# Kernel optimization log

Measured on AMD Instinct MI355X. Metric: run time of the kernel, lower is better.

The kernel has to match this reference:

```python
import jax, jax.numpy as jnp
import numpy as np

B, S, H = 64, 512, 256
H2 = 2 * H
TOPK, TRUNC = 5, 100
EPS = 1e-7
TMAX = S + 1  # h_old slot 0 is the initial zero state; one slot appended per step
NEG = -1e9


def setup_inputs() -> dict:
    key = jax.random.key(0)
    ks = jax.random.split(key, 8)
    p = lambda k, shape: jax.random.normal(k, shape, jnp.float32) * 0.08
    return {
        "x": jax.random.normal(ks[0], (B, S), jnp.float32),
        "W_ih_f": p(ks[1], (4 * H, 1)),
        "W_hh_f": p(ks[2], (4 * H, H)),
        "b_f": p(ks[3], (4 * H,)),
        "W_ih_b": p(ks[4], (4 * H, 1)),
        "W_hh_b": p(ks[5], (4 * H, H)),
        "b_b": p(ks[6], (4 * H,)),
        "w_t": p(ks[7], (4 * H, 1)),
    }


def _lstm_cell(xt, h, c, W_ih, W_hh, b):
    # torch.nn.LSTMCell: gates ordered i, f, g, o
    g = xt @ W_ih.T + h @ W_hh.T + b
    i, f, gg, o = jnp.split(g, 4, axis=1)
    i, f, o = jax.nn.sigmoid(i), jax.nn.sigmoid(f), jax.nn.sigmoid(o)
    c2 = f * c + i * jnp.tanh(gg)
    return o * jnp.tanh(c2), c2


def _forward(x, W_ih_f, W_hh_f, b_f, W_ih_b, W_hh_b, b_b, w_t):
    # tanh(cat(h_comb, h_old)) @ w_t == tanh(h_comb)@w1 + tanh(h_old)@w2
    w1, w2 = w_t[:H2, 0], w_t[H2:, 0]
    pos = jnp.arange(TMAX)

    h0 = jnp.zeros((B, H), jnp.float32)
    h_old0 = jnp.zeros((B, TMAX, H2), jnp.float32)   # slot 0 = initial zeros (valid)
    th_old0 = jnp.zeros((B, TMAX, H2), jnp.float32)  # cached tanh(h_old)
    carry0 = (h0, h0, h0, h0, h_old0, th_old0,
              jnp.zeros((B, H2), jnp.float32), jnp.zeros((B, TMAX), jnp.float32))

    def step(carry, i):
        h_f, c_f, h_b, c_b, h_old, th_old, _, _ = carry
        trunc = ((i + 1) % TRUNC) == 0  # TBPTT detach point
        sg = lambda a: jnp.where(trunc, jax.lax.stop_gradient(a), a)
        h_f, c_f, h_b, c_b = sg(h_f), sg(c_f), sg(h_b), sg(c_b)

        xf = jax.lax.dynamic_slice_in_dim(x, i, 1, axis=1)          # [B,1]
        xb = jax.lax.dynamic_slice_in_dim(x, S - 1 - i, 1, axis=1)  # [B,1]
        h_f, c_f = _lstm_cell(xf, h_f, c_f, W_ih_f, W_hh_f, b_f)
        h_b, c_b = _lstm_cell(xb, h_b, c_b, W_ih_b, W_hh_b, b_b)
        h_comb = jnp.concatenate([h_f, h_b], axis=1)  # [B,2H]

        rs = i + 1                    # remember_size before append
        valid = pos < rs              # [TMAX]
        s = jnp.tanh(h_comb) @ w1[:, None] + th_old @ w2  # [B,1]+[B,TMAX]
        s_m = jnp.where(valid[None, :], s, NEG)

        # Sparse_attention: subtract k-th largest, clamp at 0, renormalize
        delta = jax.lax.top_k(s_m, TOPK)[0][:, -1] + EPS  # [B]
        w_sp = jnp.clip(s_m - delta[:, None], 0.0, None)
        w_sp = w_sp / (w_sp.sum(axis=1, keepdims=True) + EPS)
        w_raw = jnp.where(valid[None, :], s, 0.0)  # time_step <= top_k branch
        attn_w = jnp.where(rs <= TOPK, w_raw, w_sp)  # [B,TMAX]

        attn_c = jnp.einsum('bt,bth->bh', attn_w, h_old)  # weighted sum of cache
        h_new = h_comb + attn_c

        h_old = jax.lax.dynamic_update_slice_in_dim(
            h_old, h_new[:, None, :], i + 1, axis=1)
        th_old = jax.lax.dynamic_update_slice_in_dim(
            th_old, jnp.tanh(h_new)[:, None, :], i + 1, axis=1)
        return (h_f, c_f, h_b, c_b, h_old, th_old, attn_c, attn_w), None

    carry, _ = jax.lax.scan(step, carry0, jnp.arange(S))
    attn_c, attn_w = carry[6], carry[7]
    # last step: remember_size == S, torch returns [B, S, 1]
    return attn_c, attn_w[:, :S, None]


def reference(x, W_ih_f, W_hh_f, b_f, W_ih_b, W_hh_b, b_b, w_t):
    return _forward(x, W_ih_f, W_hh_f, b_f, W_ih_b, W_hh_b, b_b, w_t)
```

## Files before the change

kernel.cpp:

```cpp
#include <hip/hip_runtime.h>
#include <math.h>

#define BB    64
#define SS    512
#define HH    256
#define HH2   512
#define TMAXX 513
#define NTOP  5
#define EPSF  1e-7f

#if defined(__has_builtin)
#if __has_builtin(__builtin_amdgcn_sdot4)
#define HAVE_SDOT4 1
#endif
#endif

__device__ __forceinline__ int dot4i8_(unsigned a, int b, int c) {
#ifdef HAVE_SDOT4
  return __builtin_amdgcn_sdot4((int)a, b, c, false);
#else
  int acc = c;
#pragma unroll
  for (int j = 0; j < 4; ++j) {
    int av = (int)(signed char)(a >> (8 * j));
    int bv = (int)(signed char)(((unsigned)b) >> (8 * j));
    acc += av * bv;
  }
  return acc;
#endif
}


__global__ void init_kernel(const float* __restrict__ Whh_f, const float* __restrict__ Whh_b,
                            uint4* __restrict__ wq, float* __restrict__ scales) {
  int t = blockIdx.x * blockDim.x + threadIdx.x;
  if (t >= 2048) return;
  int d = t >> 10, row = t & 1023;
  const float* src = (d ? Whh_b : Whh_f) + (size_t)row * HH;
  float m = 1e-20f;
  for (int k = 0; k < HH; ++k) m = fmaxf(m, fabsf(src[k]));
  float inv = 127.f / m;
  scales[t] = m * (1.f / 16129.f);
  for (int kq4 = 0; kq4 < 16; ++kq4) {
    unsigned u[4];
#pragma unroll
    for (int w = 0; w < 4; ++w) {
      unsigned uu = 0;
#pragma unroll
      for (int j = 0; j < 4; ++j) {
        float q = rintf(src[kq4 * 16 + w * 4 + j] * inv);
        q = fminf(fmaxf(q, -127.f), 127.f);
        uu |= ((unsigned)(((int)q) & 0xff)) << (8 * j);
      }
      u[w] = uu;
    }
    wq[(size_t)(d * 16 + kq4) * 1024 + row] = make_uint4(u[0], u[1], u[2], u[3]);
  }
}

__global__ __launch_bounds__(256, 1)
void lstm_kernel(const float* __restrict__ x,
                 const float* __restrict__ wihf, const float* __restrict__ bf,
                 const float* __restrict__ wihb, const float* __restrict__ bb_,
                 const uint4* __restrict__ wq, const float* __restrict__ scales,
                 float* __restrict__ hcomb) {
  const int r = blockIdx.x >> 1;
  const int d = blockIdx.x & 1;
  const int e = threadIdx.x;

  __shared__ float x_lds[SS];
  __shared__ int   hbuf[2][64];

  for (int t = e; t < SS; t += 256) x_lds[t] = x[(size_t)r * SS + t];
  if (e < 64) hbuf[0][e] = 0;

  float wih[4], bias[4], sc[4];
#pragma unroll
  for (int g = 0; g < 4; ++g) {
    int row = g * HH + e;
    wih[g]  = d ? wihb[row] : wihf[row];
    bias[g] = d ? bb_[row]  : bf[row];
    sc[g]   = scales[d * 1024 + row];
  }
  uint4 w[4][16];
#pragma unroll
  for (int g = 0; g < 4; ++g) {
    const uint4* wb = wq + (size_t)(d * 16) * 1024 + g * HH + e;
#pragma unroll
    for (int q = 0; q < 16; ++q) w[g][q] = wb[(size_t)q * 1024];
  }
  float c = 0.f;
  float* hout = hcomb + (size_t)r * SS * HH2 + d * HH;
  __syncthreads();

  int cur = 0;
  for (int i = 0; i < SS; ++i) {
    const int4* hp = (const int4*)hbuf[cur];
    int a0 = 0, a1 = 0, a2 = 0, a3 = 0;
#pragma unroll
    for (int q = 0; q < 16; ++q) {
      int4 h4 = hp[q];
      a0 = dot4i8_(w[0][q].x, h4.x, a0); a0 = dot4i8_(w[0][q].y, h4.y, a0);
      a0 = dot4i8_(w[0][q].z, h4.z, a0); a0 = dot4i8_(w[0][q].w, h4.w, a0);
      a1 = dot4i8_(w[1][q].x, h4.x, a1); a1 = dot4i8_(w[1][q].y, h4.y, a1);
      a1 = dot4i8_(w[1][q].z, h4.z, a1); a1 = dot4i8_(w[1][q].w, h4.w, a1);
      a2 = dot4i8_(w[2][q].x, h4.x, a2); a2 = dot4i8_(w[2][q].y, h4.y, a2);
      a2 = dot4i8_(w[2][q].z, h4.z, a2); a2 = dot4i8_(w[2][q].w, h4.w, a2);
      a3 = dot4i8_(w[3][q].x, h4.x, a3); a3 = dot4i8_(w[3][q].y, h4.y, a3);
      a3 = dot4i8_(w[3][q].z, h4.z, a3); a3 = dot4i8_(w[3][q].w, h4.w, a3);
    }
    float xv = x_lds[d ? (SS - 1 - i) : i];
    float gi = (float)a0 * sc[0] + fmaf(xv, wih[0], bias[0]);
    float gf = (float)a1 * sc[1] + fmaf(xv, wih[1], bias[1]);
    float gg = (float)a2 * sc[2] + fmaf(xv, wih[2], bias[2]);
    float go = (float)a3 * sc[3] + fmaf(xv, wih[3], bias[3]);
    float ig = 1.f / (1.f + expf(-gi));
    float fg = 1.f / (1.f + expf(-gf));
    float og = 1.f / (1.f + expf(-go));
    c = fg * c + ig * tanhf(gg);
    float hn = og * tanhf(c);
    hout[(size_t)i * HH2 + e] = hn;
    ((signed char*)hbuf[cur ^ 1])[e] = (signed char)(int)rintf(hn * 127.f);
    cur ^= 1;
    __syncthreads();
  }
}

__global__ __launch_bounds__(64, 1)
void attn_kernel(const float* __restrict__ w_t, const float* __restrict__ hcomb,
                 float* __restrict__ out) {
  const int b = blockIdx.x;
  const int l = threadIdx.x;
  const float* hrow = hcomb + (size_t)b * SS * HH2;

  __shared__ float tw_l[TMAXX];

  const float4 w1a = *(const float4*)(w_t + 4 * l);
  const float4 w1b = *(const float4*)(w_t + HH + 4 * l);
  const float4 w2a = *(const float4*)(w_t + HH2 + 4 * l);
  const float4 w2b = *(const float4*)(w_t + HH2 + HH + 4 * l);

  float t5v[5] = {0.f, -1e30f, -1e30f, -1e30f, -1e30f};
  int   t5s[5] = {0, 1, 2, 3, 4};
  int   t5cnt  = 1;
  float4 z4 = make_float4(0.f, 0.f, 0.f, 0.f);
  float4 sA0 = z4, sA1 = z4, sA2 = z4, sA3 = z4, sA4 = z4;
  float4 sB0 = z4, sB1 = z4, sB2 = z4, sB3 = z4, sB4 = z4;
  if (l == 0) tw_l[0] = 0.f;

  float4 ha = *(const float4*)(hrow + 4 * l);
  float4 hb = *(const float4*)(hrow + HH + 4 * l);
  float tw5 = 0.f, inv = 0.f;
  float4 aA = z4, aB = z4;

  for (int i = 0; i < SS; ++i) {
    float4 na = z4, nb = z4;
    if (i + 1 < SS) {
      na = *(const float4*)(hrow + (size_t)(i + 1) * HH2 + 4 * l);
      nb = *(const float4*)(hrow + (size_t)(i + 1) * HH2 + HH + 4 * l);
    }
    float wr[5];
    if (i >= NTOP) {
      tw5 = t5v[4];
      float rk0 = fmaxf(t5v[0] - tw5 - EPSF, 0.f);
      float rk1 = fmaxf(t5v[1] - tw5 - EPSF, 0.f);
      float rk2 = fmaxf(t5v[2] - tw5 - EPSF, 0.f);
      float rk3 = fmaxf(t5v[3] - tw5 - EPSF, 0.f);
      inv = 1.f / (rk0 + rk1 + rk2 + rk3 + EPSF);
      wr[0] = rk0 * inv; wr[1] = rk1 * inv; wr[2] = rk2 * inv; wr[3] = rk3 * inv;
      wr[4] = 0.f;
    } else {
      float s = tanhf(ha.x) * w1a.x + tanhf(ha.y) * w1a.y +
                tanhf(ha.z) * w1a.z + tanhf(ha.w) * w1a.w +
                tanhf(hb.x) * w1b.x + tanhf(hb.y) * w1b.y +
                tanhf(hb.z) * w1b.z + tanhf(hb.w) * w1b.w;
#pragma unroll
      for (int m = 1; m < 64; m <<= 1) s += __shfl_xor(s, m, 64);
#pragma unroll
      for (int k = 0; k < 5; ++k) wr[k] = (k < t5cnt) ? (s + t5v[k]) : 0.f;
    }
    float ws0 = 0.f, ws1 = 0.f, ws2 = 0.f, ws3 = 0.f, ws4 = 0.f;
#pragma unroll
    for (int k = 0; k < 5; ++k) {
      float wv = wr[k]; int s2 = t5s[k];
      ws0 += (s2 == 0) ? wv : 0.f;
      ws1 += (s2 == 1) ? wv : 0.f;
      ws2 += (s2 == 2) ? wv : 0.f;
      ws3 += (s2 == 3) ? wv : 0.f;
      ws4 += (s2 == 4) ? wv : 0.f;
    }
    aA.x = ws0*sA0.x + ws1*sA1.x + ws2*sA2.x + ws3*sA3.x + ws4*sA4.x;
    aA.y = ws0*sA0.y + ws1*sA1.y + ws2*sA2.y + ws3*sA3.y + ws4*sA4.y;
    aA.z = ws0*sA0.z + ws1*sA1.z + ws2*sA2.z + ws3*sA3.z + ws4*sA4.z;
    aA.w = ws0*sA0.w + ws1*sA1.w + ws2*sA2.w + ws3*sA3.w + ws4*sA4.w;
    aB.x = ws0*sB0.x + ws1*sB1.x + ws2*sB2.x + ws3*sB3.x + ws4*sB4.x;
    aB.y = ws0*sB0.y + ws1*sB1.y + ws2*sB2.y + ws3*sB3.y + ws4*sB4.y;
    aB.z = ws0*sB0.z + ws1*sB1.z + ws2*sB2.z + ws3*sB3.z + ws4*sB4.z;
    aB.w = ws0*sB0.w + ws1*sB1.w + ws2*sB2.w + ws3*sB3.w + ws4*sB4.w;
    float4 hnA, hnB;
    hnA.x = ha.x + aA.x; hnA.y = ha.y + aA.y; hnA.z = ha.z + aA.z; hnA.w = ha.w + aA.w;
    hnB.x = hb.x + aB.x; hnB.y = hb.y + aB.y; hnB.z = hb.z + aB.z; hnB.w = hb.w + aB.w;
    float v = tanhf(hnA.x) * w2a.x + tanhf(hnA.y) * w2a.y +
              tanhf(hnA.z) * w2a.z + tanhf(hnA.w) * w2a.w +
              tanhf(hnB.x) * w2b.x + tanhf(hnB.y) * w2b.y +
              tanhf(hnB.z) * w2b.z + tanhf(hnB.w) * w2b.w;
#pragma unroll
    for (int m = 1; m < 64; m <<= 1) v += __shfl_xor(v, m, 64);
    if (l == 0) tw_l[i + 1] = v;
    bool full = (t5cnt >= 5);
    bool ins  = !full || (v > t5v[4]);
    if (ins) {
      int p    = full ? 4 : t5cnt;
      int slot = full ? t5s[4] : t5cnt;
#pragma unroll
      for (int k = 0; k < 5; ++k) if (k == p) { t5v[k] = v; t5s[k] = slot; }
      if (slot == 0)      { sA0 = hnA; sB0 = hnB; }
      else if (slot == 1) { sA1 = hnA; sB1 = hnB; }
      else if (slot == 2) { sA2 = hnA; sB2 = hnB; }
      else if (slot == 3) { sA3 = hnA; sB3 = hnB; }
      else                { sA4 = hnA; sB4 = hnB; }
      if (!full) ++t5cnt;
#pragma unroll
      for (int k = 4; k >= 1; --k) {
        bool sw = (k <= p) && (t5v[k] > t5v[k - 1]);
        float v0 = t5v[k - 1], v1 = t5v[k];
        int   s0 = t5s[k - 1], s1 = t5s[k];
        t5v[k] = sw ? v0 : v1;  t5v[k - 1] = sw ? v1 : v0;
        t5s[k] = sw ? s0 : s1;  t5s[k - 1] = sw ? s1 : s0;
      }
    }
    ha = na; hb = nb;
  }
  *(float4*)(out + (size_t)b * HH2 + 4 * l)      = aA;
  *(float4*)(out + (size_t)b * HH2 + HH + 4 * l) = aB;
  float* ow = out + (size_t)BB * HH2 + (size_t)b * SS;
#pragma unroll
  for (int j = 0; j < 8; ++j) {
    int t = j * 64 + l;
    float rr = tw_l[t] - tw5 - EPSF;
    ow[t] = rr > 0.f ? rr * inv : 0.f;
  }
}

extern "C" void kernel_launch(void* const* d_in, const int* in_sizes, int n_in,
                              void* d_out, int out_size, void* d_ws, size_t ws_size,
                              hipStream_t stream) {
  const float* x     = (const float*)d_in[0];
  const float* Wih_f = (const float*)d_in[1];
  const float* Whh_f = (const float*)d_in[2];
  const float* b_f   = (const float*)d_in[3];
  const float* Wih_b = (const float*)d_in[4];
  const float* Whh_b = (const float*)d_in[5];
  const float* b_b   = (const float*)d_in[6];
  const float* w_t   = (const float*)d_in[7];
  float* out = (float*)d_out;

  char* ws = (char*)d_ws;
  uint4*  wq     = (uint4*)ws;
  float*  scales = (float*)(ws + (1 << 20));
  float*  hcomb  = (float*)(ws + (4 << 20));

  init_kernel<<<8, 256, 0, stream>>>(Whh_f, Whh_b, wq, scales);
  lstm_kernel<<<2 * BB, 256, 0, stream>>>(x, Wih_f, b_f, Wih_b, b_b,
                                          wq, scales, hcomb);
  attn_kernel<<<BB, 64, 0, stream>>>(w_t, hcomb, out);
}
```

Measured before the change: 1.445 ms.

## Spread LSTM gates across 1024 threads and widen attention to 512 threads

Result: faster. 1.223 ms (-15.3%).

```diff
diff --git a/kernel.cpp b/kernel.cpp
--- a/kernel.cpp
+++ b/kernel.cpp
@@ -58,36 +58,34 @@
   }
 }
 
-__global__ __launch_bounds__(256, 1)
+__global__ __launch_bounds__(1024, 4)
 void lstm_kernel(const float* __restrict__ x,
                  const float* __restrict__ wihf, const float* __restrict__ bf,
                  const float* __restrict__ wihb, const float* __restrict__ bb_,
                  const uint4* __restrict__ wq, const float* __restrict__ scales,
                  float* __restrict__ hcomb) {
-  const int r = blockIdx.x >> 1;
-  const int d = blockIdx.x & 1;
-  const int e = threadIdx.x;
+  const int r   = blockIdx.x >> 1;
+  const int d   = blockIdx.x & 1;
+  const int tid = threadIdx.x;
+  const int gate = tid >> 8;
+  const int e    = tid & 255;
 
   __shared__ float x_lds[SS];
+  __shared__ float gact[1024];
   __shared__ int   hbuf[2][64];
 
-  for (int t = e; t < SS; t += 256) x_lds[t] = x[(size_t)r * SS + t];
-  if (e < 64) hbuf[0][e] = 0;
-
-  float wih[4], bias[4], sc[4];
-#pragma unroll
-  for (int g = 0; g < 4; ++g) {
-    int row = g * HH + e;
-    wih[g]  = d ? wihb[row] : wihf[row];
-    bias[g] = d ? bb_[row]  : bf[row];
-    sc[g]   = scales[d * 1024 + row];
-  }
-  uint4 w[4][16];
-#pragma unroll
-  for (int g = 0; g < 4; ++g) {
-    const uint4* wb = wq + (size_t)(d * 16) * 1024 + g * HH + e;
-#pragma unroll
-    for (int q = 0; q < 16; ++q) w[g][q] = wb[(size_t)q * 1024];
+  for (int t = tid; t < SS; t += 1024) x_lds[t] = x[(size_t)r * SS + t];
+  if (tid < 64) hbuf[0][tid] = 0;
+
+  const float wihv = d ? wihb[tid] : wihf[tid];
+  const float bv   = d ? bb_[tid]  : bf[tid];
+  const float sc   = scales[d * 1024 + tid];
+
+  uint4 w[16];
+  {
+    const uint4* wb = wq + (size_t)(d * 16) * 1024 + tid;
+#pragma unroll
+    for (int q = 0; q < 16; ++q) w[q] = wb[(size_t)q * 1024];
   }
   float c = 0.f;
   float* hout = hcomb + (size_t)r * SS * HH2 + d * HH;
@@ -96,69 +94,61 @@
   int cur = 0;
   for (int i = 0; i < SS; ++i) {
     const int4* hp = (const int4*)hbuf[cur];
-    int a0 = 0, a1 = 0, a2 = 0, a3 = 0;
+    int a = 0;
 #pragma unroll
     for (int q = 0; q < 16; ++q) {
       int4 h4 = hp[q];
-      a0 = dot4i8_(w[0][q].x, h4.x, a0); a0 = dot4i8_(w[0][q].y, h4.y, a0);
-      a0 = dot4i8_(w[0][q].z, h4.z, a0); a0 = dot4i8_(w[0][q].w, h4.w, a0);
-      a1 = dot4i8_(w[1][q].x, h4.x, a1); a1 = dot4i8_(w[1][q].y, h4.y, a1);
-      a1 = dot4i8_(w[1][q].z, h4.z, a1); a1 = dot4i8_(w[1][q].w, h4.w, a1);
-      a2 = dot4i8_(w[2][q].x, h4.x, a2); a2 = dot4i8_(w[2][q].y, h4.y, a2);
-      a2 = dot4i8_(w[2][q].z, h4.z, a2); a2 = dot4i8_(w[2][q].w, h4.w, a2);
-      a3 = dot4i8_(w[3][q].x, h4.x, a3); a3 = dot4i8_(w[3][q].y, h4.y, a3);
-      a3 = dot4i8_(w[3][q].z, h4.z, a3); a3 = dot4i8_(w[3][q].w, h4.w, a3);
+      a = dot4i8_(w[q].x, h4.x, a);
+      a = dot4i8_(w[q].y, h4.y, a);
+      a = dot4i8_(w[q].z, h4.z, a);
+      a = dot4i8_(w[q].w, h4.w, a);
     }
     float xv = x_lds[d ? (SS - 1 - i) : i];
-    float gi = (float)a0 * sc[0] + fmaf(xv, wih[0], bias[0]);
-    float gf = (float)a1 * sc[1] + fmaf(xv, wih[1], bias[1]);
-    float gg = (float)a2 * sc[2] + fmaf(xv, wih[2], bias[2]);
-    float go = (float)a3 * sc[3] + fmaf(xv, wih[3], bias[3]);
-    float ig = 1.f / (1.f + expf(-gi));
-    float fg = 1.f / (1.f + expf(-gf));
-    float og = 1.f / (1.f + expf(-go));
-    c = fg * c + ig * tanhf(gg);
-    float hn = og * tanhf(c);
-    hout[(size_t)i * HH2 + e] = hn;
-    ((signed char*)hbuf[cur ^ 1])[e] = (signed char)(int)rintf(hn * 127.f);
+    float gv = (float)a * sc + fmaf(xv, wihv, bv);
+    gact[tid] = (gate == 2) ? tanhf(gv) : 1.f / (1.f + expf(-gv));
+    __syncthreads();
+    if (tid < HH) {
+      float ig = gact[tid];
+      float fg = gact[HH + tid];
+      float gg = gact[2 * HH + tid];
+      float og = gact[3 * HH + tid];
+      c = fg * c + ig * gg;
+      float hn = og * tanhf(c);
+      hout[(size_t)i * HH2 + tid] = hn;
+      ((signed char*)hbuf[cur ^ 1])[tid] = (signed char)(int)rintf(hn * 127.f);
+    }
     cur ^= 1;
     __syncthreads();
   }
 }
 
-__global__ __launch_bounds__(64, 1)
+__global__ __launch_bounds__(512, 1)
 void attn_kernel(const float* __restrict__ w_t, const float* __restrict__ hcomb,
                  float* __restrict__ out) {
   const int b = blockIdx.x;
-  const int l = threadIdx.x;
+  const int e = threadIdx.x;
+  const int lane = e & 63, wv = e >> 6;
   const float* hrow = hcomb + (size_t)b * SS * HH2;
 
   __shared__ float tw_l[TMAXX];
-
-  const float4 w1a = *(const float4*)(w_t + 4 * l);
-  const float4 w1b = *(const float4*)(w_t + HH + 4 * l);
-  const float4 w2a = *(const float4*)(w_t + HH2 + 4 * l);
-  const float4 w2b = *(const float4*)(w_t + HH2 + HH + 4 * l);
+  __shared__ float part[2][8];
+  __shared__ float spart[8];
+
+  const float w1e = w_t[e];
+  const float w2e = w_t[HH2 + e];
 
   float t5v[5] = {0.f, -1e30f, -1e30f, -1e30f, -1e30f};
   int   t5s[5] = {0, 1, 2, 3, 4};
   int   t5cnt  = 1;
-  float4 z4 = make_float4(0.f, 0.f, 0.f, 0.f);
-  float4 sA0 = z4, sA1 = z4, sA2 = z4, sA3 = z4, sA4 = z4;
-  float4 sB0 = z4, sB1 = z4, sB2 = z4, sB3 = z4, sB4 = z4;
-  if (l == 0) tw_l[0] = 0.f;
-
-  float4 ha = *(const float4*)(hrow + 4 * l);
-  float4 hb = *(const float4*)(hrow + HH + 4 * l);
-  float tw5 = 0.f, inv = 0.f;
-  float4 aA = z4, aB = z4;
+  float c0 = 0.f, c1 = 0.f, c2 = 0.f, c3 = 0.f, c4 = 0.f;
+  if (e == 0) tw_l[0] = 0.f;
+
+  float hc = hrow[e];
+  float tw5 = 0.f, inv = 0.f, ctx = 0.f;
+  int cur = 0;
 
   for (int i = 0; i < SS; ++i) {
-    float4 na = z4, nb = z4;
-    if (i + 1 < SS) {
-      na = *(const float4*)(hrow + (size_t)(i + 1) * HH2 + 4 * l);
-      nb = *(const float4*)(hrow + (size_t)(i + 1) * HH2 + HH + 4 * l);
-    }
+    float hc_next = (i + 1 < SS) ? hrow[(size_t)(i + 1) * HH2 + e] : 0.f;
     float wr[5];
     if (i >= NTOP) {
       tw5 = t5v[4];
@@ -170,43 +160,38 @@
       wr[0] = rk0 * inv; wr[1] = rk1 * inv; wr[2] = rk2 * inv; wr[3] = rk3 * inv;
       wr[4] = 0.f;
     } else {
-      float s = tanhf(ha.x) * w1a.x + tanhf(ha.y) * w1a.y +
-                tanhf(ha.z) * w1a.z + tanhf(ha.w) * w1a.w +
-                tanhf(hb.x) * w1b.x + tanhf(hb.y) * w1b.y +
-                tanhf(hb.z) * w1b.z + tanhf(hb.w) * w1b.w;
-#pragma unroll
-      for (int m = 1; m < 64; m <<= 1) s += __shfl_xor(s, m, 64);
+      float sv = tanhf(hc) * w1e;
+#pragma unroll
+      for (int m = 32; m >= 1; m >>= 1) sv += __shfl_xor(sv, m, 64);
+      if (lane == 0) spart[wv] = sv;
+      __syncthreads();
+      float s = spart[0] + spart[1] + spart[2] + spart[3] +
+                spart[4] + spart[5] + spart[6] + spart[7];
+      __syncthreads();
 #pragma unroll
       for (int k = 0; k < 5; ++k) wr[k] = (k < t5cnt) ? (s + t5v[k]) : 0.f;
     }
     float ws0 = 0.f, ws1 = 0.f, ws2 = 0.f, ws3 = 0.f, ws4 = 0.f;
 #pragma unroll
     for (int k = 0; k < 5; ++k) {
-      float wv = wr[k]; int s2 = t5s[k];
-      ws0 += (s2 == 0) ? wv : 0.f;
-      ws1 += (s2 == 1) ? wv : 0.f;
-      ws2 += (s2 == 2) ? wv : 0.f;
-      ws3 += (s2 == 3) ? wv : 0.f;
-      ws4 += (s2 == 4) ? wv : 0.f;
-    }
-    aA.x = ws0*sA0.x + ws1*sA1.x + ws2*sA2.x + ws3*sA3.x + ws4*sA4.x;
-    aA.y = ws0*sA0.y + ws1*sA1.y + ws2*sA2.y + ws3*sA3.y + ws4*sA4.y;
-    aA.z = ws0*sA0.z + ws1*sA1.z + ws2*sA2.z + ws3*sA3.z + ws4*sA4.z;
-    aA.w = ws0*sA0.w + ws1*sA1.w + ws2*sA2.w + ws3*sA3.w + ws4*sA4.w;
-    aB.x = ws0*sB0.x + ws1*sB1.x + ws2*sB2.x + ws3*sB3.x + ws4*sB4.x;
-    aB.y = ws0*sB0.y + ws1*sB1.y + ws2*sB2.y + ws3*sB3.y + ws4*sB4.y;
-    aB.z = ws0*sB0.z + ws1*sB1.z + ws2*sB2.z + ws3*sB3.z + ws4*sB4.z;
-    aB.w = ws0*sB0.w + ws1*sB1.w + ws2*sB2.w + ws3*sB3.w + ws4*sB4.w;
-    float4 hnA, hnB;
-    hnA.x = ha.x + aA.x; hnA.y = ha.y + aA.y; hnA.z = ha.z + aA.z; hnA.w = ha.w + aA.w;
-    hnB.x = hb.x + aB.x; hnB.y = hb.y + aB.y; hnB.z = hb.z + aB.z; hnB.w = hb.w + aB.w;
-    float v = tanhf(hnA.x) * w2a.x + tanhf(hnA.y) * w2a.y +
-              tanhf(hnA.z) * w2a.z + tanhf(hnA.w) * w2a.w +
-              tanhf(hnB.x) * w2b.x + tanhf(hnB.y) * w2b.y +
-              tanhf(hnB.z) * w2b.z + tanhf(hnB.w) * w2b.w;
-#pragma unroll
-    for (int m = 1; m < 64; m <<= 1) v += __shfl_xor(v, m, 64);
-    if (l == 0) tw_l[i + 1] = v;
+      float wvk = wr[k]; int s2 = t5s[k];
+      ws0 += (s2 == 0) ? wvk : 0.f;
+      ws1 += (s2 == 1) ? wvk : 0.f;
+      ws2 += (s2 == 2) ? wvk : 0.f;
+      ws3 += (s2 == 3) ? wvk : 0.f;
+      ws4 += (s2 == 4) ? wvk : 0.f;
+    }
+    ctx = ws0 * c0 + ws1 * c1 + ws2 * c2 + ws3 * c3 + ws4 * c4;
+    float hnew = hc + ctx;
+    float pv = tanhf(hnew) * w2e;
+#pragma unroll
+    for (int m = 32; m >= 1; m >>= 1) pv += __shfl_xor(pv, m, 64);
+    if (lane == 0) part[cur][wv] = pv;
+    __syncthreads();
+    float v = part[cur][0] + part[cur][1] + part[cur][2] + part[cur][3] +
+              part[cur][4] + part[cur][5] + part[cur][6] + part[cur][7];
+    cur ^= 1;
+    if (e == 0) tw_l[i + 1] = v;
     bool full = (t5cnt >= 5);
     bool ins  = !full || (v > t5v[4]);
     if (ins) {
@@ -214,11 +199,11 @@
       int slot = full ? t5s[4] : t5cnt;
 #pragma unroll
       for (int k = 0; k < 5; ++k) if (k == p) { t5v[k] = v; t5s[k] = slot; }
-      if (slot == 0)      { sA0 = hnA; sB0 = hnB; }
-      else if (slot == 1) { sA1 = hnA; sB1 = hnB; }
-      else if (slot == 2) { sA2 = hnA; sB2 = hnB; }
-      else if (slot == 3) { sA3 = hnA; sB3 = hnB; }
-      else                { sA4 = hnA; sB4 = hnB; }
+      c0 = (slot == 0) ? hnew : c0;
+      c1 = (slot == 1) ? hnew : c1;
+      c2 = (slot == 2) ? hnew : c2;
+      c3 = (slot == 3) ? hnew : c3;
+      c4 = (slot == 4) ? hnew : c4;
       if (!full) ++t5cnt;
 #pragma unroll
       for (int k = 4; k >= 1; --k) {
@@ -229,17 +214,12 @@
         t5s[k] = sw ? s0 : s1;  t5s[k - 1] = sw ? s1 : s0;
       }
     }
-    ha = na; hb = nb;
-  }
-  *(float4*)(out + (size_t)b * HH2 + 4 * l)      = aA;
-  *(float4*)(out + (size_t)b * HH2 + HH + 4 * l) = aB;
-  float* ow = out + (size_t)BB * HH2 + (size_t)b * SS;
-#pragma unroll
-  for (int j = 0; j < 8; ++j) {
-    int t = j * 64 + l;
-    float rr = tw_l[t] - tw5 - EPSF;
-    ow[t] = rr > 0.f ? rr * inv : 0.f;
-  }
+    hc = hc_next;
+  }
+  out[(size_t)b * HH2 + e] = ctx;
+  __syncthreads();
+  float rr = tw_l[e] - tw5 - EPSF;
+  out[(size_t)BB * HH2 + (size_t)b * SS + e] = rr > 0.f ? rr * inv : 0.f;
 }
 
 extern "C" void kernel_launch(void* const* d_in, const int* in_sizes, int n_in,
@@ -261,7 +241,7 @@
   float*  hcomb  = (float*)(ws + (4 << 20));
 
   init_kernel<<<8, 256, 0, stream>>>(Whh_f, Whh_b, wq, scales);
-  lstm_kernel<<<2 * BB, 256, 0, stream>>>(x, Wih_f, b_f, Wih_b, b_b,
-                                          wq, scales, hcomb);
-  attn_kernel<<<BB, 64, 0, stream>>>(w_t, hcomb, out);
-}
+  lstm_kernel<<<2 * BB, 1024, 0, stream>>>(x, Wih_f, b_f, Wih_b, b_b,
+                                           wq, scales, hcomb);
+  attn_kernel<<<BB, 512, 0, stream>>>(w_t, hcomb, out);
+}
```

## Split LSTM gates across 1024 threads and pipeline attention loads with DPP reductions

Applied to the files above, without the earlier changes.

New measurement: 1.356 ms. 1.07x faster.

```diff
diff --git a/kernel.cpp b/kernel.cpp
--- a/kernel.cpp
+++ b/kernel.cpp
@@ -28,6 +28,23 @@
   }
   return acc;
 #endif
+}
+
+__device__ __forceinline__ float dpp_sum64(float x) {
+  int t;
+  t = __builtin_amdgcn_update_dpp(0, __builtin_bit_cast(int, x), 0x111, 0xf, 0xf, true);
+  x += __builtin_bit_cast(float, t);
+  t = __builtin_amdgcn_update_dpp(0, __builtin_bit_cast(int, x), 0x112, 0xf, 0xf, true);
+  x += __builtin_bit_cast(float, t);
+  t = __builtin_amdgcn_update_dpp(0, __builtin_bit_cast(int, x), 0x114, 0xf, 0xe, true);
+  x += __builtin_bit_cast(float, t);
+  t = __builtin_amdgcn_update_dpp(0, __builtin_bit_cast(int, x), 0x118, 0xf, 0xc, true);
+  x += __builtin_bit_cast(float, t);
+  t = __builtin_amdgcn_update_dpp(0, __builtin_bit_cast(int, x), 0x142, 0xa, 0xf, true);
+  x += __builtin_bit_cast(float, t);
+  t = __builtin_amdgcn_update_dpp(0, __builtin_bit_cast(int, x), 0x143, 0xc, 0xf, true);
+  x += __builtin_bit_cast(float, t);
+  return __builtin_bit_cast(float, __builtin_amdgcn_readlane(__builtin_bit_cast(int, x), 63));
 }
 
 
@@ -58,37 +75,39 @@
   }
 }
 
-__global__ __launch_bounds__(256, 1)
+__global__ __launch_bounds__(1024, 4)
 void lstm_kernel(const float* __restrict__ x,
                  const float* __restrict__ wihf, const float* __restrict__ bf,
                  const float* __restrict__ wihb, const float* __restrict__ bb_,
                  const uint4* __restrict__ wq, const float* __restrict__ scales,
                  float* __restrict__ hcomb) {
-  const int r = blockIdx.x >> 1;
-  const int d = blockIdx.x & 1;
-  const int e = threadIdx.x;
+  const int r    = blockIdx.x >> 1;
+  const int d    = blockIdx.x & 1;
+  const int tid  = threadIdx.x;
+  const int gate = tid >> 8;
+  const int e    = tid & 255;
 
   __shared__ float x_lds[SS];
+  __shared__ float gact[1024];
   __shared__ int   hbuf[2][64];
 
-  for (int t = e; t < SS; t += 256) x_lds[t] = x[(size_t)r * SS + t];
-  if (e < 64) hbuf[0][e] = 0;
-
-  float wih[4], bias[4], sc[4];
-#pragma unroll
-  for (int g = 0; g < 4; ++g) {
-    int row = g * HH + e;
-    wih[g]  = d ? wihb[row] : wihf[row];
-    bias[g] = d ? bb_[row]  : bf[row];
-    sc[g]   = scales[d * 1024 + row];
-  }
-  uint4 w[4][16];
-#pragma unroll
-  for (int g = 0; g < 4; ++g) {
-    const uint4* wb = wq + (size_t)(d * 16) * 1024 + g * HH + e;
-#pragma unroll
-    for (int q = 0; q < 16; ++q) w[g][q] = wb[(size_t)q * 1024];
-  }
+  for (int t = tid; t < SS; t += 1024) x_lds[t] = x[(size_t)r * SS + t];
+  if (tid < 64) hbuf[0][tid] = 0;
+
+  const float wihv = d ? wihb[tid] : wihf[tid];
+  const float bv   = d ? bb_[tid]  : bf[tid];
+  const float sc   = scales[d * 1024 + tid];
+
+  uint4 w[16];
+  {
+    const uint4* wb = wq + (size_t)(d * 16) * 1024 + tid;
+#pragma unroll
+    for (int q = 0; q < 16; ++q) w[q] = wb[(size_t)q * 1024];
+  }
+#pragma unroll
+  for (int q = 0; q < 16; ++q)
+    asm volatile("" : "+v"(w[q].x), "+v"(w[q].y), "+v"(w[q].z), "+v"(w[q].w));
+
   float c = 0.f;
   float* hout = hcomb + (size_t)r * SS * HH2 + d * HH;
   __syncthreads();
@@ -96,31 +115,29 @@
   int cur = 0;
   for (int i = 0; i < SS; ++i) {
     const int4* hp = (const int4*)hbuf[cur];
-    int a0 = 0, a1 = 0, a2 = 0, a3 = 0;
+    int a = 0;
 #pragma unroll
     for (int q = 0; q < 16; ++q) {
       int4 h4 = hp[q];
-      a0 = dot4i8_(w[0][q].x, h4.x, a0); a0 = dot4i8_(w[0][q].y, h4.y, a0);
-      a0 = dot4i8_(w[0][q].z, h4.z, a0); a0 = dot4i8_(w[0][q].w, h4.w, a0);
-      a1 = dot4i8_(w[1][q].x, h4.x, a1); a1 = dot4i8_(w[1][q].y, h4.y, a1);
-      a1 = dot4i8_(w[1][q].z, h4.z, a1); a1 = dot4i8_(w[1][q].w, h4.w, a1);
-      a2 = dot4i8_(w[2][q].x, h4.x, a2); a2 = dot4i8_(w[2][q].y, h4.y, a2);
-      a2 = dot4i8_(w[2][q].z, h4.z, a2); a2 = dot4i8_(w[2][q].w, h4.w, a2);
-      a3 = dot4i8_(w[3][q].x, h4.x, a3); a3 = dot4i8_(w[3][q].y, h4.y, a3);
-      a3 = dot4i8_(w[3][q].z, h4.z, a3); a3 = dot4i8_(w[3][q].w, h4.w, a3);
+      a = dot4i8_(w[q].x, h4.x, a);
+      a = dot4i8_(w[q].y, h4.y, a);
+      a = dot4i8_(w[q].z, h4.z, a);
+      a = dot4i8_(w[q].w, h4.w, a);
     }
     float xv = x_lds[d ? (SS - 1 - i) : i];
-    float gi = (float)a0 * sc[0] + fmaf(xv, wih[0], bias[0]);
-    float gf = (float)a1 * sc[1] + fmaf(xv, wih[1], bias[1]);
-    float gg = (float)a2 * sc[2] + fmaf(xv, wih[2], bias[2]);
-    float go = (float)a3 * sc[3] + fmaf(xv, wih[3], bias[3]);
-    float ig = 1.f / (1.f + expf(-gi));
-    float fg = 1.f / (1.f + expf(-gf));
-    float og = 1.f / (1.f + expf(-go));
-    c = fg * c + ig * tanhf(gg);
+    float gv = (float)a * sc + fmaf(xv, wihv, bv);
+    gact[tid] = (gate == 2) ? tanhf(gv) : 1.f / (1.f + expf(-gv));
+    __syncthreads();
+    float ig = gact[e];
+    float fg = gact[HH + e];
+    float gg = gact[2 * HH + e];
+    float og = gact[3 * HH + e];
+    c = fg * c + ig * gg;
     float hn = og * tanhf(c);
-    hout[(size_t)i * HH2 + e] = hn;
-    ((signed char*)hbuf[cur ^ 1])[e] = (signed char)(int)rintf(hn * 127.f);
+    if (gate == 0) {
+      hout[(size_t)i * HH2 + e] = hn;
+      ((signed char*)hbuf[cur ^ 1])[e] = (signed char)(int)rintf(hn * 127.f);
+    }
     cur ^= 1;
     __syncthreads();
   }
@@ -148,17 +165,18 @@
   float4 sB0 = z4, sB1 = z4, sB2 = z4, sB3 = z4, sB4 = z4;
   if (l == 0) tw_l[0] = 0.f;
 
-  float4 ha = *(const float4*)(hrow + 4 * l);
-  float4 hb = *(const float4*)(hrow + HH + 4 * l);
   float tw5 = 0.f, inv = 0.f;
-  float4 aA = z4, aB = z4;
-
-  for (int i = 0; i < SS; ++i) {
-    float4 na = z4, nb = z4;
-    if (i + 1 < SS) {
-      na = *(const float4*)(hrow + (size_t)(i + 1) * HH2 + 4 * l);
-      nb = *(const float4*)(hrow + (size_t)(i + 1) * HH2 + HH + 4 * l);
-    }
+
+  float4 a0 = *(const float4*)(hrow + 0 * HH2 + 4 * l);
+  float4 b0 = *(const float4*)(hrow + 0 * HH2 + HH + 4 * l);
+  float4 a1 = *(const float4*)(hrow + 1 * HH2 + 4 * l);
+  float4 b1 = *(const float4*)(hrow + 1 * HH2 + HH + 4 * l);
+  float4 a2 = *(const float4*)(hrow + 2 * HH2 + 4 * l);
+  float4 b2 = *(const float4*)(hrow + 2 * HH2 + HH + 4 * l);
+  float4 a3 = *(const float4*)(hrow + 3 * HH2 + 4 * l);
+  float4 b3 = *(const float4*)(hrow + 3 * HH2 + HH + 4 * l);
+
+  auto step = [&](float4& ha, float4& hb, int i) {
     float wr[5];
     if (i >= NTOP) {
       tw5 = t5v[4];
@@ -170,12 +188,11 @@
       wr[0] = rk0 * inv; wr[1] = rk1 * inv; wr[2] = rk2 * inv; wr[3] = rk3 * inv;
       wr[4] = 0.f;
     } else {
-      float s = tanhf(ha.x) * w1a.x + tanhf(ha.y) * w1a.y +
-                tanhf(ha.z) * w1a.z + tanhf(ha.w) * w1a.w +
-                tanhf(hb.x) * w1b.x + tanhf(hb.y) * w1b.y +
-                tanhf(hb.z) * w1b.z + tanhf(hb.w) * w1b.w;
-#pragma unroll
-      for (int m = 1; m < 64; m <<= 1) s += __shfl_xor(s, m, 64);
+      float sv = tanhf(ha.x) * w1a.x + tanhf(ha.y) * w1a.y +
+                 tanhf(ha.z) * w1a.z + tanhf(ha.w) * w1a.w +
+                 tanhf(hb.x) * w1b.x + tanhf(hb.y) * w1b.y +
+                 tanhf(hb.z) * w1b.z + tanhf(hb.w) * w1b.w;
+      float s = dpp_sum64(sv);
 #pragma unroll
       for (int k = 0; k < 5; ++k) wr[k] = (k < t5cnt) ? (s + t5v[k]) : 0.f;
     }
@@ -189,24 +206,36 @@
       ws3 += (s2 == 3) ? wv : 0.f;
       ws4 += (s2 == 4) ? wv : 0.f;
     }
-    aA.x = ws0*sA0.x + ws1*sA1.x + ws2*sA2.x + ws3*sA3.x + ws4*sA4.x;
-    aA.y = ws0*sA0.y + ws1*sA1.y + ws2*sA2.y + ws3*sA3.y + ws4*sA4.y;
-    aA.z = ws0*sA0.z + ws1*sA1.z + ws2*sA2.z + ws3*sA3.z + ws4*sA4.z;
-    aA.w = ws0*sA0.w + ws1*sA1.w + ws2*sA2.w + ws3*sA3.w + ws4*sA4.w;
-    aB.x = ws0*sB0.x + ws1*sB1.x + ws2*sB2.x + ws3*sB3.x + ws4*sB4.x;
-    aB.y = ws0*sB0.y + ws1*sB1.y + ws2*sB2.y + ws3*sB3.y + ws4*sB4.y;
-    aB.z = ws0*sB0.z + ws1*sB1.z + ws2*sB2.z + ws3*sB3.z + ws4*sB4.z;
-    aB.w = ws0*sB0.w + ws1*sB1.w + ws2*sB2.w + ws3*sB3.w + ws4*sB4.w;
+    float4 cxA, cxB;
+    cxA.x = ws0*sA0.x + ws1*sA1.x + ws2*sA2.x + ws3*sA3.x + ws4*sA4.x;
+    cxA.y = ws0*sA0.y + ws1*sA1.y + ws2*sA2.y + ws3*sA3.y + ws4*sA4.y;
+    cxA.z = ws0*sA0.z + ws1*sA1.z + ws2*sA2.z + ws3*sA3.z + ws4*sA4.z;
+    cxA.w = ws0*sA0.w + ws1*sA1.w + ws2*sA2.w + ws3*sA3.w + ws4*sA4.w;
+    cxB.x = ws0*sB0.x + ws1*sB1.x + ws2*sB2.x + ws3*sB3.x + ws4*sB4.x;
+    cxB.y = ws0*sB0.y + ws1*sB1.y + ws2*sB2.y + ws3*sB3.y + ws4*sB4.y;
+    cxB.z = ws0*sB0.z + ws1*sB1.z + ws2*sB2.z + ws3*sB3.z + ws4*sB4.z;
+    cxB.w = ws0*sB0.w + ws1*sB1.w + ws2*sB2.w + ws3*sB3.w + ws4*sB4.w;
     float4 hnA, hnB;
-    hnA.x = ha.x + aA.x; hnA.y = ha.y + aA.y; hnA.z = ha.z + aA.z; hnA.w = ha.w + aA.w;
-    hnB.x = hb.x + aB.x; hnB.y = hb.y + aB.y; hnB.z = hb.z + aB.z; hnB.w = hb.w + aB.w;
-    float v = tanhf(hnA.x) * w2a.x + tanhf(hnA.y) * w2a.y +
-              tanhf(hnA.z) * w2a.z + tanhf(hnA.w) * w2a.w +
-              tanhf(hnB.x) * w2b.x + tanhf(hnB.y) * w2b.y +
-              tanhf(hnB.z) * w2b.z + tanhf(hnB.w) * w2b.w;
-#pragma unroll
-    for (int m = 1; m < 64; m <<= 1) v += __shfl_xor(v, m, 64);
+    hnA.x = ha.x + cxA.x; hnA.y = ha.y + cxA.y; hnA.z = ha.z + cxA.z; hnA.w = ha.w + cxA.w;
+    hnB.x = hb.x + cxB.x; hnB.y = hb.y + cxB.y; hnB.z = hb.z + cxB.z; hnB.w = hb.w + cxB.w;
+    float pv = tanhf(hnA.x) * w2a.x + tanhf(hnA.y) * w2a.y +
+               tanhf(hnA.z) * w2a.z + tanhf(hnA.w) * w2a.w +
+               tanhf(hnB.x) * w2b.x + tanhf(hnB.y) * w2b.y +
+               tanhf(hnB.z) * w2b.z + tanhf(hnB.w) * w2b.w;
+    float v = dpp_sum64(pv);
     if (l == 0) tw_l[i + 1] = v;
+    if (i == SS - 1) {
+      *(float4*)(out + (size_t)b * HH2 + 4 * l)      = cxA;
+      *(float4*)(out + (size_t)b * HH2 + HH + 4 * l) = cxB;
+      float* ow = out + (size_t)BB * HH2 + (size_t)b * SS;
+#pragma unroll
+      for (int j = 0; j < 8; ++j) {
+        int t = j * 64 + l;
+        float rr = tw_l[t] - tw5 - EPSF;
+        ow[t] = rr > 0.f ? rr * inv : 0.f;
+      }
+      return;
+    }
     bool full = (t5cnt >= 5);
     bool ins  = !full || (v > t5v[4]);
     if (ins) {
@@ -229,16 +258,17 @@
         t5s[k] = sw ? s0 : s1;  t5s[k - 1] = sw ? s1 : s0;
       }
     }
-    ha = na; hb = nb;
-  }
-  *(float4*)(out + (size_t)b * HH2 + 4 * l)      = aA;
-  *(float4*)(out + (size_t)b * HH2 + HH + 4 * l) = aB;
-  float* ow = out + (size_t)BB * HH2 + (size_t)b * SS;
-#pragma unroll
-  for (int j = 0; j < 8; ++j) {
-    int t = j * 64 + l;
-    float rr = tw_l[t] - tw5 - EPSF;
-    ow[t] = rr > 0.f ? rr * inv : 0.f;
+    if (i + 4 < SS) {
+      ha = *(const float4*)(hrow + (size_t)(i + 4) * HH2 + 4 * l);
+      hb = *(const float4*)(hrow + (size_t)(i + 4) * HH2 + HH + 4 * l);
+    }
+  };
+
+  for (int i = 0; i < SS; i += 4) {
+    step(a0, b0, i);
+    step(a1, b1, i + 1);
+    step(a2, b2, i + 2);
+    step(a3, b3, i + 3);
   }
 }
 
@@ -261,7 +291,7 @@
   float*  hcomb  = (float*)(ws + (4 << 20));
 
   init_kernel<<<8, 256, 0, stream>>>(Whh_f, Whh_b, wq, scales);
-  lstm_kernel<<<2 * BB, 256, 0, stream>>>(x, Wih_f, b_f, Wih_b, b_b,
-                                          wq, scales, hcomb);
+  lstm_kernel<<<2 * BB, 1024, 0, stream>>>(x, Wih_f, b_f, Wih_b, b_b,
+                                           wq, scales, hcomb);
   attn_kernel<<<BB, 64, 0, stream>>>(w_t, hcomb, out);
 }
```
